# Optimization experiments

Measured on AMD Instinct MI355X. Metric: run time of the kernel, lower is better.

The kernel has to match this reference:

```python
import jax, jax.numpy as jnp
import numpy as np

D_MODEL = 256
N_LAYERS = 8
NUM_CLASSES = 3
INPUT_DIM = 1
BATCH = 8
SEQ = 2048
EXIT_IDX = (1, 3, 5, 7)  # n_layers//4-1, n_layers//2-1, 3n//4-1, n-1
LN_EPS = 1e-5


def setup_inputs() -> dict:
    key = jax.random.key(0)
    ks = jax.random.split(key, 16)
    d, nl, nc = D_MODEL, N_LAYERS, NUM_CLASSES
    return {
        "x": jax.random.normal(ks[0], (BATCH, SEQ, INPUT_DIM), jnp.float32),
        "in_W": jax.random.normal(ks[1], (d, INPUT_DIM), jnp.float32) * 0.02,
        "in_b": jnp.zeros((d,), jnp.float32),
        "A_params": jax.random.normal(ks[2], (nl, d), jnp.float32) * 0.1,
        "B_params": jax.random.normal(ks[3], (nl, d), jnp.float32),
        "C_params": jax.random.normal(ks[4], (nl, d), jnp.float32),
        "D_params": jax.random.normal(ks[5], (nl, d), jnp.float32),
        "proj_W": jax.random.normal(ks[6], (nl, d, d), jnp.float32) * 0.02,
        "proj_b": jnp.zeros((nl, d), jnp.float32),
        "ln_g": jnp.ones((nl, d), jnp.float32),
        "ln_b": jnp.zeros((nl, d), jnp.float32),
        "head_W": jax.random.normal(ks[7], (4, nc, d), jnp.float32) * 0.02,
        "head_b": jnp.zeros((4, nc), jnp.float32),
    }


def _ssm_block(x, Ap, Bp, Cp, Dp, pW, pb, g, b):
    # x: [B, L, d]
    Bsz, L, d = x.shape
    A = jax.nn.sigmoid(Ap)                               # [d]
    t = jnp.arange(L, dtype=jnp.float32)
    K = (Cp[:, None] * (A[:, None] ** t[None, :]) * Bp[:, None])[:, None, :]  # [d,1,L]
    xt = jnp.swapaxes(x, 1, 2)                           # [B, d, L]
    # torch F.conv1d(pad=L-1, groups=d) then [..., :L] == left-pad-only cross-correlation
    out = jax.lax.conv_general_dilated(
        xt, K, window_strides=(1,), padding=[(L - 1, 0)], feature_group_count=d
    )                                                    # [B, d, L]
    out = out + Dp[None, :, None] * xt
    out = jnp.swapaxes(out, 1, 2)                        # [B, L, d]
    out = jax.nn.gelu(out, approximate=False) @ pW.T + pb
    y = x + out
    mu = jnp.mean(y, axis=-1, keepdims=True)
    var = jnp.var(y, axis=-1, keepdims=True)
    return (y - mu) / jnp.sqrt(var + LN_EPS) * g + b


def reference(x, in_W, in_b, A_params, B_params, C_params, D_params,
              proj_W, proj_b, ln_g, ln_b, head_W, head_b):
    h = x @ in_W.T + in_b                                # [B, L, d]
    logits = []
    head = 0
    for i in range(N_LAYERS):
        h = _ssm_block(h, A_params[i], B_params[i], C_params[i], D_params[i],
                       proj_W[i], proj_b[i], ln_g[i], ln_b[i])
        if i in EXIT_IDX:
            pooled = jnp.mean(h, axis=1)                 # [B, d]
            logits.append(pooled @ head_W[head].T + head_b[head])
            head += 1
    return jnp.stack(logits, axis=0)                     # [4, B, num_classes]
```

## Files before the change

### kernel.cpp

```cpp
#include <hip/hip_runtime.h>
#include <math.h>

#define DM 256
#define LSEQ 2048
#define BATCH 8
#define NLAYER 8
#define EMAX 192
#define LN_EPS 1e-5f
#define BM 32
#define BLKS 64
#define NPROD 7
#define TAILB 57

#define AL_OFF   16384
#define RED_OFF  32768
#define SMEM_SZ  (RED_OFF + 1280)

typedef float f32x4 __attribute__((ext_vector_type(4)));
typedef short bf16x8 __attribute__((ext_vector_type(8)));
typedef unsigned short u16;
typedef unsigned short u16x8 __attribute__((ext_vector_type(8)));

union V8 { u16x8 u; bf16x8 b; };

__device__ __forceinline__ float erf_fast(float x) {
    float ax = fabsf(x);
    float t = __builtin_amdgcn_rcpf(fmaf(0.3275911f, ax, 1.f));
    float p = fmaf(t, 1.061405429f, -1.453152027f);
    p = fmaf(t, p, 1.421413741f);
    p = fmaf(t, p, -0.284496736f);
    p = fmaf(t, p, 0.254829592f);
    p = p * t;
    float e = __expf(-ax * ax);
    float r = 1.f - p * e;
    return copysignf(r, x);
}

__device__ __forceinline__ float gelu_fast(float v) {
    return 0.5f * v * (1.f + erf_fast(v * 0.70710678118654752f));
}

__device__ __forceinline__ void split2(float g, u16& hi, u16& lo) {
    unsigned u = __float_as_uint(g);
    hi = (u16)(u >> 16);
    float fh = __uint_as_float(u & 0xFFFF0000u);
    float r = g - fh;
    unsigned v = __float_as_uint(r);
    v = v + 0x7FFFu + ((v >> 16) & 1u);
    lo = (u16)(v >> 16);
}

__device__ __forceinline__ void writeA(char* smem, int row, int col, u16 hi, u16 lo) {
    int aby = row * 512 + (((col >> 3) ^ (row & 7)) << 4) + (col & 7) * 2;
    *(u16*)(smem + aby) = hi;
    *(u16*)(smem + AL_OFF + aby) = lo;
}

__global__ void k_prep(const float* __restrict__ pW, u16* __restrict__ pWh,
                       u16* __restrict__ pWl,
                       const float* __restrict__ x, const float* __restrict__ inW,
                       const float* __restrict__ inb, const float* __restrict__ Ap,
                       const float* __restrict__ Bp, const float* __restrict__ Cp,
                       float* __restrict__ P_all, float* __restrict__ logA_all,
                       float* __restrict__ CB_all, float* __restrict__ pooled,
                       int* __restrict__ flags) {
    if (blockIdx.x < 256) {
        int i = blockIdx.x * 256 + threadIdx.x;
        int e = i * 8;
        int l = e >> 16;
        int r = e & 65535;
        int cg = r >> 12;
        int ks = (r >> 9) & 7;
        int lane = (r >> 3) & 63;
        int fq = lane >> 4, fr = lane & 15;
        int col = (cg >> 2) * 64 + (cg & 3) * 16 + fr;
        int k = ks * 32 + fq * 8;
        const float* src = pW + l * 65536 + col * 256 + k;
        float4 w0 = *(const float4*)src;
        float4 w1 = *(const float4*)(src + 4);
        float vv[8] = {w0.x, w0.y, w0.z, w0.w, w1.x, w1.y, w1.z, w1.w};
        u16 sh[8], sl[8];
#pragma unroll
        for (int j = 0; j < 8; ++j) split2(vv[j], sh[j], sl[j]);
        u16x8 vh = {sh[0], sh[1], sh[2], sh[3], sh[4], sh[5], sh[6], sh[7]};
        u16x8 vl = {sl[0], sl[1], sl[2], sl[3], sl[4], sl[5], sl[6], sl[7]};
        *(u16x8*)&pWh[e] = vh;
        *(u16x8*)&pWl[e] = vl;
    } else {
        int b = blockIdx.x - 256;
        int c = threadIdx.x;
        float A0 = 1.f / (1.f + expf(-Ap[c]));
        float iw = inW[c], ib = inb[c];
        const float* xb = x + b * LSEQ;
        float pw = 1.f, acc = 0.f;
        for (int t = 0; t <= EMAX; ++t) {
            acc += (xb[t] * iw + ib) * pw;
            pw *= A0;
        }
        P_all[b * DM + c] = acc;
        for (int l = 1; l < NLAYER; ++l) P_all[l * BATCH * DM + b * DM + c] = 0.f;
        for (int e = 0; e < 4; ++e) pooled[e * BATCH * DM + b * DM + c] = 0.f;
        if (b == 0) {
            for (int l = 0; l < NLAYER; ++l) {
                float Al = 1.f / (1.f + expf(-Ap[l * DM + c]));
                logA_all[l * DM + c] = logf(Al);
                CB_all[l * DM + c]   = Bp[l * DM + c] * Cp[l * DM + c];
            }
            if (c < NLAYER * BATCH) flags[c] = 0;
        }
    }
}

__global__ __launch_bounds__(256, 2) void k_fused(
    const float* __restrict__ x, const float* __restrict__ inW,
    const float* __restrict__ inb,
    const u16* __restrict__ pWh, const u16* __restrict__ pWl,
    const float* __restrict__ Dp_all, const float* __restrict__ pb_all,
    const float* __restrict__ lng_all, const float* __restrict__ lnb_all,
    const float* __restrict__ logA_all, const float* __restrict__ CB_all,
    float* __restrict__ P_all, float* __restrict__ pooled,
    int* __restrict__ flags)
{
    __shared__ __align__(16) char smem[SMEM_SZ];

    int tid  = threadIdx.x;
    int lane = tid & 63;
    int wn   = tid >> 6;
    int fr   = lane & 15;
    int fq   = lane >> 4;

    int b    = blockIdx.x >> 6;
    int blk  = blockIdx.x & 63;
    int brow = b * LSEQ + blk * BM;
    bool isTail = (blk >= TAILB);
    bool isProd = (blk < NPROD);

    int cols[4];
#pragma unroll
    for (int n = 0; n < 4; ++n) cols[n] = wn * 64 + n * 16 + fr;

    float hreg[2][4][4];

    {
        float wiv[4], biv[4], D0v[4];
#pragma unroll
        for (int n = 0; n < 4; ++n) {
            wiv[n] = inW[cols[n]];
            biv[n] = inb[cols[n]];
            D0v[n] = Dp_all[cols[n]];
        }
        float la0[4], cb0[4], P0[4];
        if (isTail) {
#pragma unroll
            for (int n = 0; n < 4; ++n) {
                la0[n] = logA_all[cols[n]];
                cb0[n] = CB_all[cols[n]];
                P0[n]  = P_all[b * DM + cols[n]];
            }
        }
#pragma unroll
        for (int m = 0; m < 2; ++m)
#pragma unroll
            for (int r = 0; r < 4; ++r) {
                int row = m * 16 + fq * 4 + r;
                float xv = x[brow + row];
                int u = (LSEQ - 1) - ((brow + row) & (LSEQ - 1));
                bool tl = isTail && (u <= EMAX);
                float uf = (float)u;
#pragma unroll
                for (int n = 0; n < 4; ++n) {
                    float h0 = fmaf(xv, wiv[n], biv[n]);
                    hreg[m][n][r] = h0;
                    float v = D0v[n] * h0;
                    if (tl) v += cb0[n] * __expf(uf * la0[n]) * P0[n];
                    u16 hi, lo;
                    split2(gelu_fast(v), hi, lo);
                    writeA(smem, row, cols[n], hi, lo);
                }
            }
    }
    __syncthreads();

    for (int l = 0; l < NLAYER; ++l) {
        f32x4 acc[2][4];
#pragma unroll
        for (int m = 0; m < 2; ++m)
#pragma unroll
            for (int n = 0; n < 4; ++n) acc[m][n] = (f32x4){0.f, 0.f, 0.f, 0.f};

        const u16* bhp = pWh + (size_t)l * 65536 + wn * 16384 + lane * 8;
        const u16* blp = pWl + (size_t)l * 65536 + wn * 16384 + lane * 8;

        V8 bhd[3][4], bld[3][4];
#pragma unroll
        for (int n = 0; n < 4; ++n) {
            bhd[0][n].u = *(const u16x8*)&bhp[n * 4096];
            bld[0][n].u = *(const u16x8*)&blp[n * 4096];
            bhd[1][n].u = *(const u16x8*)&bhp[n * 4096 + 512];
            bld[1][n].u = *(const u16x8*)&blp[n * 4096 + 512];
        }
#pragma unroll
        for (int ks = 0; ks < 8; ++ks) {
            int cur = ks % 3;
            if (ks < 6) {
                int nx2 = (ks + 2) % 3;
#pragma unroll
                for (int n = 0; n < 4; ++n) {
                    bhd[nx2][n].u = *(const u16x8*)&bhp[n * 4096 + (ks + 2) * 512];
                    bld[nx2][n].u = *(const u16x8*)&blp[n * 4096 + (ks + 2) * 512];
                }
            }
            V8 ah[2], al[2];
#pragma unroll
            for (int m = 0; m < 2; ++m) {
                int row = m * 16 + fr;
                int aby = row * 512 + (((ks * 4 + fq) ^ (row & 7)) << 4);
                ah[m].u = *(const u16x8*)(smem + aby);
                al[m].u = *(const u16x8*)(smem + AL_OFF + aby);
            }
#pragma unroll
            for (int m = 0; m < 2; ++m)
#pragma unroll
                for (int n = 0; n < 4; ++n) {
                    acc[m][n] = __builtin_amdgcn_mfma_f32_16x16x32_bf16(ah[m].b, bhd[cur][n].b, acc[m][n], 0, 0, 0);
                    acc[m][n] = __builtin_amdgcn_mfma_f32_16x16x32_bf16(ah[m].b, bld[cur][n].b, acc[m][n], 0, 0, 0);
                    acc[m][n] = __builtin_amdgcn_mfma_f32_16x16x32_bf16(al[m].b, bhd[cur][n].b, acc[m][n], 0, 0, 0);
                }
        }

        float pbv[4], lgv[4], lbv[4];
#pragma unroll
        for (int n = 0; n < 4; ++n) {
            pbv[n] = pb_all[l * DM + cols[n]];
            lgv[n] = lng_all[l * DM + cols[n]];
            lbv[n] = lnb_all[l * DM + cols[n]];
        }
        float s[2][4], ss[2][4];
#pragma unroll
        for (int m = 0; m < 2; ++m)
#pragma unroll
            for (int r = 0; r < 4; ++r) {
                float sy = 0.f, sy2 = 0.f;
#pragma unroll
                for (int n = 0; n < 4; ++n) {
                    float y = hreg[m][n][r] + acc[m][n][r] + pbv[n];
                    acc[m][n][r] = y;
                    sy += y; sy2 += y * y;
                }
                s[m][r] = sy; ss[m][r] = sy2;
            }
#pragma unroll
        for (int m = 0; m < 2; ++m)
#pragma unroll
            for (int r = 0; r < 4; ++r)
#pragma unroll
                for (int msk = 1; msk < 16; msk <<= 1) {
                    s[m][r]  += __shfl_xor(s[m][r],  msk);
                    ss[m][r] += __shfl_xor(ss[m][r], msk);
                }
        if (fr == 0) {
#pragma unroll
            for (int m = 0; m < 2; ++m)
#pragma unroll
                for (int r = 0; r < 4; ++r) {
                    int row = m * 16 + fq * 4 + r;
                    *(float*)(smem + RED_OFF + (row * 10 + wn * 2)     * 4) = s[m][r];
                    *(float*)(smem + RED_OFF + (row * 10 + wn * 2 + 1) * 4) = ss[m][r];
                }
        }
        __syncthreads();

        float mean[2][4], rstd[2][4];
#pragma unroll
        for (int m = 0; m < 2; ++m)
#pragma unroll
            for (int r = 0; r < 4; ++r) {
                int row = m * 16 + fq * 4 + r;
                float st = 0.f, sst = 0.f;
#pragma unroll
                for (int w = 0; w < 4; ++w) {
                    st  += *(const float*)(smem + RED_OFF + (row * 10 + w * 2)     * 4);
                    sst += *(const float*)(smem + RED_OFF + (row * 10 + w * 2 + 1) * 4);
                }
                float mu = st * (1.f / 256.f);
                float var = sst * (1.f / 256.f) - mu * mu;
                mean[m][r] = mu;
                rstd[m][r] = rsqrtf(var + LN_EPS);
            }
        int slot = (l == 1) ? 0 : (l == 3) ? 1 : (l == 5) ? 2 : (l == 7) ? 3 : -1;
        bool last = (l == NLAYER - 1);
        bool prod = !last && isProd;
        float Dnv[4], lanv[4];
        if (!last) {
#pragma unroll
            for (int n = 0; n < 4; ++n) Dnv[n] = Dp_all[(l + 1) * DM + cols[n]];
        }
        if (prod) {
#pragma unroll
            for (int n = 0; n < 4; ++n) lanv[n] = logA_all[(l + 1) * DM + cols[n]];
        }
        float cs[4] = {0.f, 0.f, 0.f, 0.f};
        float pc[4] = {0.f, 0.f, 0.f, 0.f};
#pragma unroll
        for (int m = 0; m < 2; ++m)
#pragma unroll
            for (int r = 0; r < 4; ++r) {
                int row  = m * 16 + fq * 4 + r;
                int trow = blk * BM + row;
#pragma unroll
                for (int n = 0; n < 4; ++n) {
                    float o = (acc[m][n][r] - mean[m][r]) * rstd[m][r] * lgv[n] + lbv[n];
                    hreg[m][n][r] = o;
                    if (!last) {
                        u16 hi, lo;
                        split2(gelu_fast(Dnv[n] * o), hi, lo);
                        writeA(smem, row, cols[n], hi, lo);
                    }
                    if (slot >= 0) cs[n] += o;
                    if (prod && trow <= EMAX) pc[n] += o * __expf((float)trow * lanv[n]);
                }
            }
        if (slot >= 0) {
#pragma unroll
            for (int n = 0; n < 4; ++n) {
                cs[n] += __shfl_xor(cs[n], 16);
                cs[n] += __shfl_xor(cs[n], 32);
            }
            if (lane < 16) {
#pragma unroll
                for (int n = 0; n < 4; ++n)
                    atomicAdd(&pooled[slot * (BATCH * DM) + b * DM + wn * 64 + n * 16 + lane], cs[n]);
            }
        }
        if (prod) {
#pragma unroll
            for (int n = 0; n < 4; ++n) {
                pc[n] += __shfl_xor(pc[n], 16);
                pc[n] += __shfl_xor(pc[n], 32);
            }
            if (lane < 16) {
#pragma unroll
                for (int n = 0; n < 4; ++n)
                    atomicAdd(&P_all[(size_t)(l + 1) * BATCH * DM + b * DM + wn * 64 + n * 16 + lane], pc[n]);
            }
        }
        __syncthreads();

        if (!last) {
            if (prod && tid == 0)
                __hip_atomic_fetch_add(&flags[(l + 1) * BATCH + b], 1,
                                       __ATOMIC_RELEASE, __HIP_MEMORY_SCOPE_AGENT);
            if (isTail) {
                if (tid == 0) {
                    while (__hip_atomic_load(&flags[(l + 1) * BATCH + b], __ATOMIC_ACQUIRE,
                                             __HIP_MEMORY_SCOPE_AGENT) < NPROD)
                        __builtin_amdgcn_s_sleep(2);
                }
                __syncthreads();
                float lanx[4], cbnx[4], Pnx[4];
#pragma unroll
                for (int n = 0; n < 4; ++n) {
                    lanx[n] = logA_all[(l + 1) * DM + cols[n]];
                    cbnx[n] = CB_all[(l + 1) * DM + cols[n]];
                    Pnx[n]  = __hip_atomic_load(
                        &P_all[(size_t)(l + 1) * BATCH * DM + b * DM + cols[n]],
                        __ATOMIC_RELAXED, __HIP_MEMORY_SCOPE_AGENT);
                }
#pragma unroll
                for (int m = 0; m < 2; ++m)
#pragma unroll
                    for (int r = 0; r < 4; ++r) {
                        int row = m * 16 + fq * 4 + r;
                        int u = (LSEQ - 1) - ((brow + row) & (LSEQ - 1));
                        if (u <= EMAX) {
                            float uf = (float)u;
#pragma unroll
                            for (int n = 0; n < 4; ++n) {
                                float v = Dnv[n] * hreg[m][n][r] +
                                          cbnx[n] * __expf(uf * lanx[n]) * Pnx[n];
                                u16 hi, lo;
                                split2(gelu_fast(v), hi, lo);
                                writeA(smem, row, cols[n], hi, lo);
                            }
                        }
                    }
                __syncthreads();
            }
        }
    }
}

__global__ void k_head(const float* __restrict__ pooled, const float* __restrict__ hW,
                       const float* __restrict__ hb, float* __restrict__ out) {
    int tid = threadIdx.x;
    if (tid >= 96) return;
    int e = tid / 24;
    int r = tid % 24;
    int b = r / 3;
    int n = r % 3;
    const float* pv = &pooled[e * (BATCH * DM) + b * DM];
    const float* wv = &hW[(e * 3 + n) * DM];
    float acc = 0.f;
    for (int c = 0; c < DM; ++c) acc += pv[c] * wv[c];
    out[e * 24 + b * 3 + n] = acc * (1.f / (float)LSEQ) + hb[e * 3 + n];
}

extern "C" void kernel_launch(void* const* d_in, const int* in_sizes, int n_in,
                              void* d_out, int out_size, void* d_ws, size_t ws_size,
                              hipStream_t stream) {
    const float* x   = (const float*)d_in[0];
    const float* inW = (const float*)d_in[1];
    const float* inb = (const float*)d_in[2];
    const float* Ap  = (const float*)d_in[3];
    const float* Bp  = (const float*)d_in[4];
    const float* Cp  = (const float*)d_in[5];
    const float* Dp  = (const float*)d_in[6];
    const float* pW  = (const float*)d_in[7];
    const float* pb  = (const float*)d_in[8];
    const float* lng = (const float*)d_in[9];
    const float* lnb = (const float*)d_in[10];
    const float* hW  = (const float*)d_in[11];
    const float* hb  = (const float*)d_in[12];
    float* out = (float*)d_out;

    float* ws = (float*)d_ws;
    float* P_all    = ws;
    float* logA_all = P_all + NLAYER * BATCH * DM;
    float* CB_all   = logA_all + NLAYER * DM;
    float* pooled   = CB_all + NLAYER * DM;
    u16* pWh        = (u16*)(pooled + 4 * BATCH * DM);
    u16* pWl        = pWh + NLAYER * DM * DM;
    int* flags      = (int*)(pWl + NLAYER * DM * DM);

    k_prep<<<264, 256, 0, stream>>>(pW, pWh, pWl, x, inW, inb, Ap, Bp, Cp,
                                    P_all, logA_all, CB_all, pooled, flags);
    k_fused<<<BATCH * BLKS, 256, 0, stream>>>(
        x, inW, inb, pWh, pWl, Dp, pb, lng, lnb,
        logA_all, CB_all, P_all, pooled, flags);
    k_head<<<1, 128, 0, stream>>>(pooled, hW, hb, out);
}
```

Measured before the change: 147.4 us.

## Halve row tile to 16, double block count, remap columns for vector LDS stores

Shrinks each block's row tile from 32 to 16 rows, so there are twice as many blocks (128 per batch). The producer and tail block counts are adjusted to match, and launch bounds rise to 4 blocks per CU for more occupancy. The column mapping is permuted so each lane owns 4 contiguous columns. This turns global and LDS accesses into float4 and u16x4 vector operations, and the weight layout in prep changes to match. The first k-slice of the next layer's weights is now prefetched before the barrier, using a 2-stage buffer instead of 3. The trade-off is that weight fragments are reused over fewer rows, so each block does twice as much global weight traffic per output row.

```diff
diff --git a/kernel.cpp b/kernel.cpp
--- a/kernel.cpp
+++ b/kernel.cpp
@@ -7,18 +7,19 @@
 #define NLAYER 8
 #define EMAX 192
 #define LN_EPS 1e-5f
-#define BM 32
-#define BLKS 64
-#define NPROD 7
-#define TAILB 57
-
-#define AL_OFF   16384
-#define RED_OFF  32768
-#define SMEM_SZ  (RED_OFF + 1280)
+#define BM 16
+#define BLKS 128
+#define NPROD 13
+#define TAILB 115
+
+#define AL_OFF  8192
+#define RED_OFF 16384
+#define SMEM_SZ (RED_OFF + 640)
 
 typedef float f32x4 __attribute__((ext_vector_type(4)));
 typedef short bf16x8 __attribute__((ext_vector_type(8)));
 typedef unsigned short u16;
+typedef unsigned short u16x4 __attribute__((ext_vector_type(4)));
 typedef unsigned short u16x8 __attribute__((ext_vector_type(8)));
 
 union V8 { u16x8 u; bf16x8 b; };
@@ -50,10 +51,9 @@
     lo = (u16)(v >> 16);
 }
 
-__device__ __forceinline__ void writeA(char* smem, int row, int col, u16 hi, u16 lo) {
-    int aby = row * 512 + (((col >> 3) ^ (row & 7)) << 4) + (col & 7) * 2;
-    *(u16*)(smem + aby) = hi;
-    *(u16*)(smem + AL_OFF + aby) = lo;
+__device__ __forceinline__ int a_addr(int row, int wn, int fr) {
+    int unit = wn * 8 + (fr >> 1);
+    return row * 512 + ((unit ^ (row & 7)) << 4) + (fr & 1) * 8;
 }
 
 __global__ void k_prep(const float* __restrict__ pW, u16* __restrict__ pWh,
@@ -73,7 +73,7 @@
         int ks = (r >> 9) & 7;
         int lane = (r >> 3) & 63;
         int fq = lane >> 4, fr = lane & 15;
-        int col = (cg >> 2) * 64 + (cg & 3) * 16 + fr;
+        int col = (cg >> 2) * 64 + fr * 4 + (cg & 3);
         int k = ks * 32 + fq * 8;
         const float* src = pW + l * 65536 + col * 256 + k;
         float4 w0 = *(const float4*)src;
@@ -111,7 +111,7 @@
     }
 }
 
-__global__ __launch_bounds__(256, 2) void k_fused(
+__global__ __launch_bounds__(256, 4) void k_fused(
     const float* __restrict__ x, const float* __restrict__ inW,
     const float* __restrict__ inb,
     const u16* __restrict__ pWh, const u16* __restrict__ pWl,
@@ -129,197 +129,184 @@
     int fr   = lane & 15;
     int fq   = lane >> 4;
 
-    int b    = blockIdx.x >> 6;
-    int blk  = blockIdx.x & 63;
+    int b    = blockIdx.x >> 7;
+    int blk  = blockIdx.x & 127;
     int brow = b * LSEQ + blk * BM;
     bool isTail = (blk >= TAILB);
     bool isProd = (blk < NPROD);
 
-    int cols[4];
-#pragma unroll
-    for (int n = 0; n < 4; ++n) cols[n] = wn * 64 + n * 16 + fr;
-
-    float hreg[2][4][4];
+    int col0 = wn * 64 + fr * 4;
+    float hreg[4][4];
 
     {
-        float wiv[4], biv[4], D0v[4];
+        float4 wi = *(const float4*)&inW[col0];
+        float4 bi = *(const float4*)&inb[col0];
+        float4 d0 = *(const float4*)&Dp_all[col0];
+        float4 la0, cb0, P0;
+        if (isTail) {
+            la0 = *(const float4*)&logA_all[col0];
+            cb0 = *(const float4*)&CB_all[col0];
+            P0  = *(const float4*)&P_all[b * DM + col0];
+        }
+#pragma unroll
+        for (int r = 0; r < 4; ++r) {
+            int row = fq * 4 + r;
+            int gr  = brow + row;
+            float xv = x[gr];
+            int u = (LSEQ - 1) - (gr & (LSEQ - 1));
+            bool tl = isTail && (u <= EMAX);
+            float uf = (float)u;
+            float v[4];
+            v[0] = fmaf(xv, wi.x, bi.x); hreg[0][r] = v[0];
+            v[1] = fmaf(xv, wi.y, bi.y); hreg[1][r] = v[1];
+            v[2] = fmaf(xv, wi.z, bi.z); hreg[2][r] = v[2];
+            v[3] = fmaf(xv, wi.w, bi.w); hreg[3][r] = v[3];
+            v[0] *= d0.x; v[1] *= d0.y; v[2] *= d0.z; v[3] *= d0.w;
+            if (tl) {
+                v[0] += cb0.x * __expf(uf * la0.x) * P0.x;
+                v[1] += cb0.y * __expf(uf * la0.y) * P0.y;
+                v[2] += cb0.z * __expf(uf * la0.z) * P0.z;
+                v[3] += cb0.w * __expf(uf * la0.w) * P0.w;
+            }
+            u16 sh[4], sl[4];
+#pragma unroll
+            for (int n = 0; n < 4; ++n) split2(gelu_fast(v[n]), sh[n], sl[n]);
+            u16x4 vh = {sh[0], sh[1], sh[2], sh[3]};
+            u16x4 vl = {sl[0], sl[1], sl[2], sl[3]};
+            int aby = a_addr(row, wn, fr);
+            *(u16x4*)(smem + aby) = vh;
+            *(u16x4*)(smem + AL_OFF + aby) = vl;
+        }
+    }
+
+    V8 bhd[2][4], bld[2][4];
+    {
+        const u16* bhp0 = pWh + wn * 16384 + lane * 8;
+        const u16* blp0 = pWl + wn * 16384 + lane * 8;
 #pragma unroll
         for (int n = 0; n < 4; ++n) {
-            wiv[n] = inW[cols[n]];
-            biv[n] = inb[cols[n]];
-            D0v[n] = Dp_all[cols[n]];
-        }
-        float la0[4], cb0[4], P0[4];
-        if (isTail) {
-#pragma unroll
-            for (int n = 0; n < 4; ++n) {
-                la0[n] = logA_all[cols[n]];
-                cb0[n] = CB_all[cols[n]];
-                P0[n]  = P_all[b * DM + cols[n]];
-            }
-        }
-#pragma unroll
-        for (int m = 0; m < 2; ++m)
-#pragma unroll
-            for (int r = 0; r < 4; ++r) {
-                int row = m * 16 + fq * 4 + r;
-                float xv = x[brow + row];
-                int u = (LSEQ - 1) - ((brow + row) & (LSEQ - 1));
-                bool tl = isTail && (u <= EMAX);
-                float uf = (float)u;
-#pragma unroll
-                for (int n = 0; n < 4; ++n) {
-                    float h0 = fmaf(xv, wiv[n], biv[n]);
-                    hreg[m][n][r] = h0;
-                    float v = D0v[n] * h0;
-                    if (tl) v += cb0[n] * __expf(uf * la0[n]) * P0[n];
-                    u16 hi, lo;
-                    split2(gelu_fast(v), hi, lo);
-                    writeA(smem, row, cols[n], hi, lo);
-                }
-            }
+            bhd[0][n].u = *(const u16x8*)&bhp0[n * 4096];
+            bld[0][n].u = *(const u16x8*)&blp0[n * 4096];
+        }
     }
     __syncthreads();
 
     for (int l = 0; l < NLAYER; ++l) {
-        f32x4 acc[2][4];
-#pragma unroll
-        for (int m = 0; m < 2; ++m)
-#pragma unroll
-            for (int n = 0; n < 4; ++n) acc[m][n] = (f32x4){0.f, 0.f, 0.f, 0.f};
-
         const u16* bhp = pWh + (size_t)l * 65536 + wn * 16384 + lane * 8;
         const u16* blp = pWl + (size_t)l * 65536 + wn * 16384 + lane * 8;
 
-        V8 bhd[3][4], bld[3][4];
-#pragma unroll
-        for (int n = 0; n < 4; ++n) {
-            bhd[0][n].u = *(const u16x8*)&bhp[n * 4096];
-            bld[0][n].u = *(const u16x8*)&blp[n * 4096];
-            bhd[1][n].u = *(const u16x8*)&bhp[n * 4096 + 512];
-            bld[1][n].u = *(const u16x8*)&blp[n * 4096 + 512];
-        }
+        f32x4 acc[4];
+#pragma unroll
+        for (int n = 0; n < 4; ++n) acc[n] = (f32x4){0.f, 0.f, 0.f, 0.f};
+
 #pragma unroll
         for (int ks = 0; ks < 8; ++ks) {
-            int cur = ks % 3;
-            if (ks < 6) {
-                int nx2 = (ks + 2) % 3;
+            int cur = ks & 1, nxt = cur ^ 1;
+            if (ks < 7) {
 #pragma unroll
                 for (int n = 0; n < 4; ++n) {
-                    bhd[nx2][n].u = *(const u16x8*)&bhp[n * 4096 + (ks + 2) * 512];
-                    bld[nx2][n].u = *(const u16x8*)&blp[n * 4096 + (ks + 2) * 512];
+                    bhd[nxt][n].u = *(const u16x8*)&bhp[n * 4096 + (ks + 1) * 512];
+                    bld[nxt][n].u = *(const u16x8*)&blp[n * 4096 + (ks + 1) * 512];
                 }
             }
-            V8 ah[2], al[2];
-#pragma unroll
-            for (int m = 0; m < 2; ++m) {
-                int row = m * 16 + fr;
-                int aby = row * 512 + (((ks * 4 + fq) ^ (row & 7)) << 4);
-                ah[m].u = *(const u16x8*)(smem + aby);
-                al[m].u = *(const u16x8*)(smem + AL_OFF + aby);
-            }
-#pragma unroll
-            for (int m = 0; m < 2; ++m)
-#pragma unroll
-                for (int n = 0; n < 4; ++n) {
-                    acc[m][n] = __builtin_amdgcn_mfma_f32_16x16x32_bf16(ah[m].b, bhd[cur][n].b, acc[m][n], 0, 0, 0);
-                    acc[m][n] = __builtin_amdgcn_mfma_f32_16x16x32_bf16(ah[m].b, bld[cur][n].b, acc[m][n], 0, 0, 0);
-                    acc[m][n] = __builtin_amdgcn_mfma_f32_16x16x32_bf16(al[m].b, bhd[cur][n].b, acc[m][n], 0, 0, 0);
-                }
-        }
-
-        float pbv[4], lgv[4], lbv[4];
-#pragma unroll
-        for (int n = 0; n < 4; ++n) {
-            pbv[n] = pb_all[l * DM + cols[n]];
-            lgv[n] = lng_all[l * DM + cols[n]];
-            lbv[n] = lnb_all[l * DM + cols[n]];
-        }
-        float s[2][4], ss[2][4];
-#pragma unroll
-        for (int m = 0; m < 2; ++m)
+            V8 ah, al;
+            {
+                int aby = fr * 512 + (((ks * 4 + fq) ^ (fr & 7)) << 4);
+                ah.u = *(const u16x8*)(smem + aby);
+                al.u = *(const u16x8*)(smem + AL_OFF + aby);
+            }
+#pragma unroll
+            for (int n = 0; n < 4; ++n) {
+                acc[n] = __builtin_amdgcn_mfma_f32_16x16x32_bf16(ah.b, bhd[cur][n].b, acc[n], 0, 0, 0);
+                acc[n] = __builtin_amdgcn_mfma_f32_16x16x32_bf16(ah.b, bld[cur][n].b, acc[n], 0, 0, 0);
+                acc[n] = __builtin_amdgcn_mfma_f32_16x16x32_bf16(al.b, bhd[cur][n].b, acc[n], 0, 0, 0);
+            }
+        }
+
+        float4 pbv = *(const float4*)&pb_all[l * DM + col0];
+        float4 lgv = *(const float4*)&lng_all[l * DM + col0];
+        float4 lbv = *(const float4*)&lnb_all[l * DM + col0];
+        float s[4], ss[4];
+#pragma unroll
+        for (int r = 0; r < 4; ++r) {
+            float y0 = hreg[0][r] + acc[0][r] + pbv.x;
+            float y1 = hreg[1][r] + acc[1][r] + pbv.y;
+            float y2 = hreg[2][r] + acc[2][r] + pbv.z;
+            float y3 = hreg[3][r] + acc[3][r] + pbv.w;
+            acc[0][r] = y0; acc[1][r] = y1; acc[2][r] = y2; acc[3][r] = y3;
+            s[r]  = y0 + y1 + y2 + y3;
+            ss[r] = y0 * y0 + y1 * y1 + y2 * y2 + y3 * y3;
+        }
+#pragma unroll
+        for (int r = 0; r < 4; ++r)
+#pragma unroll
+            for (int msk = 1; msk < 16; msk <<= 1) {
+                s[r]  += __shfl_xor(s[r],  msk);
+                ss[r] += __shfl_xor(ss[r], msk);
+            }
+        if (fr == 0) {
 #pragma unroll
             for (int r = 0; r < 4; ++r) {
-                float sy = 0.f, sy2 = 0.f;
-#pragma unroll
-                for (int n = 0; n < 4; ++n) {
-                    float y = hreg[m][n][r] + acc[m][n][r] + pbv[n];
-                    acc[m][n][r] = y;
-                    sy += y; sy2 += y * y;
-                }
-                s[m][r] = sy; ss[m][r] = sy2;
-            }
-#pragma unroll
-        for (int m = 0; m < 2; ++m)
-#pragma unroll
-            for (int r = 0; r < 4; ++r)
-#pragma unroll
-                for (int msk = 1; msk < 16; msk <<= 1) {
-                    s[m][r]  += __shfl_xor(s[m][r],  msk);
-                    ss[m][r] += __shfl_xor(ss[m][r], msk);
-                }
-        if (fr == 0) {
-#pragma unroll
-            for (int m = 0; m < 2; ++m)
-#pragma unroll
-                for (int r = 0; r < 4; ++r) {
-                    int row = m * 16 + fq * 4 + r;
-                    *(float*)(smem + RED_OFF + (row * 10 + wn * 2)     * 4) = s[m][r];
-                    *(float*)(smem + RED_OFF + (row * 10 + wn * 2 + 1) * 4) = ss[m][r];
-                }
+                int row = fq * 4 + r;
+                *(float*)(smem + RED_OFF + (row * 10 + wn * 2)     * 4) = s[r];
+                *(float*)(smem + RED_OFF + (row * 10 + wn * 2 + 1) * 4) = ss[r];
+            }
         }
         __syncthreads();
 
-        float mean[2][4], rstd[2][4];
-#pragma unroll
-        for (int m = 0; m < 2; ++m)
-#pragma unroll
-            for (int r = 0; r < 4; ++r) {
-                int row = m * 16 + fq * 4 + r;
-                float st = 0.f, sst = 0.f;
-#pragma unroll
-                for (int w = 0; w < 4; ++w) {
-                    st  += *(const float*)(smem + RED_OFF + (row * 10 + w * 2)     * 4);
-                    sst += *(const float*)(smem + RED_OFF + (row * 10 + w * 2 + 1) * 4);
-                }
-                float mu = st * (1.f / 256.f);
-                float var = sst * (1.f / 256.f) - mu * mu;
-                mean[m][r] = mu;
-                rstd[m][r] = rsqrtf(var + LN_EPS);
-            }
+        float mean[4], rstd[4];
+#pragma unroll
+        for (int r = 0; r < 4; ++r) {
+            int row = fq * 4 + r;
+            float st = 0.f, sst = 0.f;
+#pragma unroll
+            for (int w = 0; w < 4; ++w) {
+                st  += *(const float*)(smem + RED_OFF + (row * 10 + w * 2)     * 4);
+                sst += *(const float*)(smem + RED_OFF + (row * 10 + w * 2 + 1) * 4);
+            }
+            float mu = st * (1.f / 256.f);
+            float var = sst * (1.f / 256.f) - mu * mu;
+            mean[r] = mu;
+            rstd[r] = rsqrtf(var + LN_EPS);
+        }
         int slot = (l == 1) ? 0 : (l == 3) ? 1 : (l == 5) ? 2 : (l == 7) ? 3 : -1;
         bool last = (l == NLAYER - 1);
         bool prod = !last && isProd;
-        float Dnv[4], lanv[4];
-        if (!last) {
-#pragma unroll
-            for (int n = 0; n < 4; ++n) Dnv[n] = Dp_all[(l + 1) * DM + cols[n]];
-        }
-        if (prod) {
-#pragma unroll
-            for (int n = 0; n < 4; ++n) lanv[n] = logA_all[(l + 1) * DM + cols[n]];
-        }
+        float4 Dnv, lanv;
+        if (!last) Dnv = *(const float4*)&Dp_all[(l + 1) * DM + col0];
+        if (prod)  lanv = *(const float4*)&logA_all[(l + 1) * DM + col0];
         float cs[4] = {0.f, 0.f, 0.f, 0.f};
         float pc[4] = {0.f, 0.f, 0.f, 0.f};
 #pragma unroll
-        for (int m = 0; m < 2; ++m)
-#pragma unroll
-            for (int r = 0; r < 4; ++r) {
-                int row  = m * 16 + fq * 4 + r;
-                int trow = blk * BM + row;
-#pragma unroll
-                for (int n = 0; n < 4; ++n) {
-                    float o = (acc[m][n][r] - mean[m][r]) * rstd[m][r] * lgv[n] + lbv[n];
-                    hreg[m][n][r] = o;
-                    if (!last) {
-                        u16 hi, lo;
-                        split2(gelu_fast(Dnv[n] * o), hi, lo);
-                        writeA(smem, row, cols[n], hi, lo);
-                    }
-                    if (slot >= 0) cs[n] += o;
-                    if (prod && trow <= EMAX) pc[n] += o * __expf((float)trow * lanv[n]);
-                }
-            }
+        for (int r = 0; r < 4; ++r) {
+            int row  = fq * 4 + r;
+            int trow = blk * BM + row;
+            float o0 = (acc[0][r] - mean[r]) * rstd[r] * lgv.x + lbv.x;
+            float o1 = (acc[1][r] - mean[r]) * rstd[r] * lgv.y + lbv.y;
+            float o2 = (acc[2][r] - mean[r]) * rstd[r] * lgv.z + lbv.z;
+            float o3 = (acc[3][r] - mean[r]) * rstd[r] * lgv.w + lbv.w;
+            hreg[0][r] = o0; hreg[1][r] = o1; hreg[2][r] = o2; hreg[3][r] = o3;
+            if (slot >= 0) { cs[0] += o0; cs[1] += o1; cs[2] += o2; cs[3] += o3; }
+            if (prod && trow <= EMAX) {
+                float tf = (float)trow;
+                pc[0] += o0 * __expf(tf * lanv.x);
+                pc[1] += o1 * __expf(tf * lanv.y);
+                pc[2] += o2 * __expf(tf * lanv.z);
+                pc[3] += o3 * __expf(tf * lanv.w);
+            }
+            if (!last) {
+                u16 sh[4], sl[4];
+                split2(gelu_fast(Dnv.x * o0), sh[0], sl[0]);
+                split2(gelu_fast(Dnv.y * o1), sh[1], sl[1]);
+                split2(gelu_fast(Dnv.z * o2), sh[2], sl[2]);
+                split2(gelu_fast(Dnv.w * o3), sh[3], sl[3]);
+                u16x4 vh = {sh[0], sh[1], sh[2], sh[3]};
+                u16x4 vl = {sl[0], sl[1], sl[2], sl[3]};
+                int aby = a_addr(row, wn, fr);
+                *(u16x4*)(smem + aby) = vh;
+                *(u16x4*)(smem + AL_OFF + aby) = vl;
+            }
+        }
         if (slot >= 0) {
 #pragma unroll
             for (int n = 0; n < 4; ++n) {
@@ -329,7 +316,7 @@
             if (lane < 16) {
 #pragma unroll
                 for (int n = 0; n < 4; ++n)
-                    atomicAdd(&pooled[slot * (BATCH * DM) + b * DM + wn * 64 + n * 16 + lane], cs[n]);
+                    atomicAdd(&pooled[slot * (BATCH * DM) + b * DM + wn * 64 + lane * 4 + n], cs[n]);
             }
         }
         if (prod) {
@@ -341,7 +328,17 @@
             if (lane < 16) {
 #pragma unroll
                 for (int n = 0; n < 4; ++n)
-                    atomicAdd(&P_all[(size_t)(l + 1) * BATCH * DM + b * DM + wn * 64 + n * 16 + lane], pc[n]);
+                    atomicAdd(&P_all[(size_t)(l + 1) * BATCH * DM + b * DM + wn * 64 + lane * 4 + n], pc[n]);
+            }
+        }
+
+        if (!last) {
+            const u16* bhpN = pWh + (size_t)(l + 1) * 65536 + wn * 16384 + lane * 8;
+            const u16* blpN = pWl + (size_t)(l + 1) * 65536 + wn * 16384 + lane * 8;
+#pragma unroll
+            for (int n = 0; n < 4; ++n) {
+                bhd[0][n].u = *(const u16x8*)&bhpN[n * 4096];
+                bld[0][n].u = *(const u16x8*)&blpN[n * 4096];
             }
         }
         __syncthreads();
@@ -357,33 +354,36 @@
                         __builtin_amdgcn_s_sleep(2);
                 }
                 __syncthreads();
-                float lanx[4], cbnx[4], Pnx[4];
-#pragma unroll
-                for (int n = 0; n < 4; ++n) {
-                    lanx[n] = logA_all[(l + 1) * DM + cols[n]];
-                    cbnx[n] = CB_all[(l + 1) * DM + cols[n]];
-                    Pnx[n]  = __hip_atomic_load(
-                        &P_all[(size_t)(l + 1) * BATCH * DM + b * DM + cols[n]],
+                float4 lanx = *(const float4*)&logA_all[(l + 1) * DM + col0];
+                float4 cbnx = *(const float4*)&CB_all[(l + 1) * DM + col0];
+                float Pn[4];
+#pragma unroll
+                for (int n = 0; n < 4; ++n)
+                    Pn[n] = __hip_atomic_load(
+                        &P_all[(size_t)(l + 1) * BATCH * DM + b * DM + col0 + n],
                         __ATOMIC_RELAXED, __HIP_MEMORY_SCOPE_AGENT);
+                float lan[4] = {lanx.x, lanx.y, lanx.z, lanx.w};
+                float cbn[4] = {cbnx.x, cbnx.y, cbnx.z, cbnx.w};
+                float Dn[4]  = {Dnv.x, Dnv.y, Dnv.z, Dnv.w};
+#pragma unroll
+                for (int r = 0; r < 4; ++r) {
+                    int row = fq * 4 + r;
+                    int u = (LSEQ - 1) - ((brow + row) & (LSEQ - 1));
+                    if (u <= EMAX) {
+                        float uf = (float)u;
+                        u16 sh[4], sl[4];
+#pragma unroll
+                        for (int n = 0; n < 4; ++n) {
+                            float v = Dn[n] * hreg[n][r] + cbn[n] * __expf(uf * lan[n]) * Pn[n];
+                            split2(gelu_fast(v), sh[n], sl[n]);
+                        }
+                        u16x4 vh = {sh[0], sh[1], sh[2], sh[3]};
+                        u16x4 vl = {sl[0], sl[1], sl[2], sl[3]};
+                        int aby = a_addr(row, wn, fr);
+                        *(u16x4*)(smem + aby) = vh;
+                        *(u16x4*)(smem + AL_OFF + aby) = vl;
+                    }
                 }
-#pragma unroll
-                for (int m = 0; m < 2; ++m)
-#pragma unroll
-                    for (int r = 0; r < 4; ++r) {
-                        int row = m * 16 + fq * 4 + r;
-                        int u = (LSEQ - 1) - ((brow + row) & (LSEQ - 1));
-                        if (u <= EMAX) {
-                            float uf = (float)u;
-#pragma unroll
-                            for (int n = 0; n < 4; ++n) {
-                                float v = Dnv[n] * hreg[m][n][r] +
-                                          cbnx[n] * __expf(uf * lanx[n]) * Pnx[n];
-                                u16 hi, lo;
-                                split2(gelu_fast(v), hi, lo);
-                                writeA(smem, row, cols[n], hi, lo);
-                            }
-                        }
-                    }
                 __syncthreads();
             }
         }
```

Result: slower. 207.8 us (+40.9%).
